# Kernel optimization log

Measured on AMD Instinct MI355X. Metric: run time of the kernel, lower is better.

Reference implementation:

```python
import jax, jax.numpy as jnp
import numpy as np

B, L, C, R, DK = 8, 2048, 512, 64, 64
H = 2 * C  # hdnSize
NEG = -32767.0  # -2**15 + 1
EPS = 1e-5


def _p(key, shape, std=0.02):
    return (jax.random.normal(key, shape, dtype=jnp.float32) * std)


def setup_inputs() -> dict:
    key = jax.random.key(0)
    ks = jax.random.split(key, 16)
    inp = {
        "x": jax.random.normal(ks[0], (B, L, C), dtype=jnp.float32),
        "maskPAD": jax.random.randint(ks[1], (B, 1, L), 0, 2, dtype=jnp.int32),
        "preScores": jax.random.normal(ks[2], (B, R, R), dtype=jnp.float32),
        "Wp": _p(ks[3], (C, R)), "bp": jnp.zeros((R,), jnp.float32),
        "Wq": _p(ks[4], (C, DK)), "bq": jnp.zeros((DK,), jnp.float32),
        "Wk": _p(ks[5], (C, DK)), "bk": jnp.zeros((DK,), jnp.float32),
        "Wv": _p(ks[6], (C, H)), "bv": jnp.zeros((H,), jnp.float32),
        "Wu": _p(ks[7], (C, H)), "bu": jnp.zeros((H,), jnp.float32),
        "Wo": _p(ks[8], (H, C)), "bo": jnp.zeros((C,), jnp.float32),
        "gamma": jnp.ones((C,), jnp.float32),
        "beta": jnp.zeros((C,), jnp.float32),
    }
    return inp


def reference(x, maskPAD, preScores, Wp, bp, Wq, bq, Wk, bk, Wv, bv, Wu, bu, Wo, bo, gamma, beta):
    # GLU gate: [B,L,H]
    gate = jax.nn.silu(x @ Wu + bu)
    # pseudo-attention logits [B,L,r], masked on padded positions
    pScore = x @ Wp + bp
    pad = (maskPAD[:, 0] == 0)[..., None]  # [B,L,1]
    pScore = jnp.where(pad, NEG, pScore)
    pAlpha = jax.nn.softmax(pScore, axis=1)    # softmax over L (dim=-2)
    pAlpha_ = jax.nn.softmax(pScore, axis=-1)  # softmax over r
    # compress: px [B,r,C]  (== pAlpha.transpose(-1,-2) @ x)
    px = jnp.einsum('blr,blc->brc', pAlpha, x)
    q = jax.nn.silu(px @ Wq + bq)  # [B,r,dk]
    k = jax.nn.silu(px @ Wk + bk)  # [B,r,dk]
    v = jax.nn.silu(px @ Wv + bv)  # [B,r,H]
    scores = jnp.einsum('brd,bsd->brs', q, k) / np.sqrt(DK).astype(np.float32)
    scores = scores + preScores
    alpha = jax.nn.softmax(scores, axis=2)
    z = alpha @ v                                # [B,r,H]
    z = jnp.einsum('blr,brh->blh', pAlpha_, z)   # expand back to [B,L,H]
    z = gate * z
    z = z @ Wo + bo                              # [B,L,C]
    y = x + z
    mu = jnp.mean(y, axis=-1, keepdims=True)
    var = jnp.var(y, axis=-1, keepdims=True)
    out = (y - mu) * jax.lax.rsqrt(var + EPS) * gamma + beta
    return out
```

## Files before the change

### kernel.cpp

```cpp
#include <hip/hip_runtime.h>
#include <hip/hip_bf16.h>

constexpr int B_ = 8;
constexpr int L_ = 2048;
constexpr int C_ = 512;
constexpr int R_ = 64;
constexpr int DK_ = 64;
constexpr int H_ = 1024;
constexpr int M_ = B_ * L_;
constexpr int NQKV_ = 1152;
constexpr float NEG_ = -32767.0f;

__device__ __forceinline__ float toF(float x) { return x; }
__device__ __forceinline__ float toF(__hip_bfloat16 x) { return __bfloat162float(x); }
__device__ __forceinline__ float siluf(float v) { return v / (1.0f + __expf(-v)); }
__device__ __forceinline__ ushort bfbits(float f) {
    __hip_bfloat16 h = __float2bfloat16(f);
    union { __hip_bfloat16 h; ushort u; } cv; cv.h = h; return cv.u;
}
__device__ __forceinline__ float bf2f(ushort u) {
    union { uint u; float f; } cv; cv.u = (uint)u << 16; return cv.f;
}

typedef __attribute__((ext_vector_type(8))) short bf16x8;
typedef __attribute__((ext_vector_type(4))) float f32x4;

#define GLOBAL_AS __attribute__((address_space(1)))
#define LDS_AS    __attribute__((address_space(3)))
__device__ __forceinline__ void glds16(const ushort* g, ushort* l) {
    __builtin_amdgcn_global_load_lds((const GLOBAL_AS void*)g, (LDS_AS void*)l, 16, 0, 0);
}

#define VMCNT(n) asm volatile("s_waitcnt vmcnt(" #n ")" ::: "memory")
#define BARRIER() do { __builtin_amdgcn_s_barrier(); asm volatile("" ::: "memory"); } while (0)

template <int EPI>
__global__ __launch_bounds__(256) void mfma_gemm5(
    const ushort* __restrict__ A, const ushort* __restrict__ Bt,
    const float* __restrict__ bias,
    const float* __restrict__ residF, const ushort* __restrict__ residB,
    const int* __restrict__ mask,
    ushort* __restrict__ outB, float* __restrict__ outF, float* __restrict__ outF2,
    int Ndim, int Kdim, int gridN, long bBatch)
{
    __shared__ ushort As[3][128 * 32];
    __shared__ ushort Bs[3][128 * 32];

    const int i = blockIdx.x;
    const int G = gridDim.x >> 3;
    const int gi = (gridDim.x & 7) ? i : ((i & 7) * G + (i >> 3));
    const int nt = gi % gridN, mt = gi / gridN;
    const int m0 = mt * 128, n0 = nt * 128;

    const int tid = threadIdx.x;
    const int lane = tid & 63, w = tid >> 6;
    const int wm = (w & 1) * 64, wn = (w >> 1) * 64;
    const int lr = lane & 15, lq = lane >> 4;

    const int sr = lane >> 2;
    const int sc = (lane & 3) * 8;
    const int s0 = w * 2, s1 = w * 2 + 1;

    const ushort* Bp = Bt + (bBatch ? (long)(m0 / L_) * bBatch : 0);
    int br0 = n0 + s0 * 16 + sr; if (br0 >= Ndim) br0 = Ndim - 1;
    int br1 = n0 + s1 * 16 + sr; if (br1 >= Ndim) br1 = Ndim - 1;
    const ushort* a0p = A  + (size_t)(m0 + s0 * 16 + sr) * Kdim + sc;
    const ushort* a1p = A  + (size_t)(m0 + s1 * 16 + sr) * Kdim + sc;
    const ushort* b0p = Bp + (size_t)br0 * Kdim + sc;
    const ushort* b1p = Bp + (size_t)br1 * Kdim + sc;
    const int lo0 = s0 * 512 + lane * 8;
    const int lo1 = s1 * 512 + lane * 8;

    f32x4 acc[4][4];
#pragma unroll
    for (int a = 0; a < 4; ++a)
#pragma unroll
        for (int b = 0; b < 4; ++b) acc[a][b] = (f32x4){0.f, 0.f, 0.f, 0.f};

    glds16(a0p, &As[0][lo0]);
    glds16(a1p, &As[0][lo1]);
    glds16(b0p, &Bs[0][lo0]);
    glds16(b1p, &Bs[0][lo1]);
    if (32 < Kdim) {
        glds16(a0p + 32, &As[1][lo0]);
        glds16(a1p + 32, &As[1][lo1]);
        glds16(b0p + 32, &Bs[1][lo0]);
        glds16(b1p + 32, &Bs[1][lo1]);
    }

    int cur = 0;
    for (int k0 = 0; k0 < Kdim; k0 += 32) {
        if (k0 + 32 < Kdim) VMCNT(4); else VMCNT(0);
        BARRIER();
        if (k0 + 64 < Kdim) {
            const int nx = cur ? cur - 1 : 2;
            glds16(a0p + k0 + 64, &As[nx][lo0]);
            glds16(a1p + k0 + 64, &As[nx][lo1]);
            glds16(b0p + k0 + 64, &Bs[nx][lo0]);
            glds16(b1p + k0 + 64, &Bs[nx][lo1]);
        }
        bf16x8 af[4], bf[4];
#pragma unroll
        for (int a = 0; a < 4; ++a)
            af[a] = *(const bf16x8*)&As[cur][(wm + a * 16 + lr) * 32 + lq * 8];
#pragma unroll
        for (int b = 0; b < 4; ++b)
            bf[b] = *(const bf16x8*)&Bs[cur][(wn + b * 16 + lr) * 32 + lq * 8];
#pragma unroll
        for (int a = 0; a < 4; ++a)
#pragma unroll
            for (int b = 0; b < 4; ++b)
                acc[a][b] = __builtin_amdgcn_mfma_f32_16x16x32_bf16(af[a], bf[b], acc[a][b], 0, 0, 0);
        cur = (cur == 2) ? 0 : cur + 1;
    }

#pragma unroll
    for (int a = 0; a < 4; ++a) {
#pragma unroll
        for (int b = 0; b < 4; ++b) {
            const int col = n0 + wn + b * 16 + lr;
            if (col < Ndim) {
                const float bn = (EPI == 3) ? 0.f : bias[col];
#pragma unroll
                for (int r = 0; r < 4; ++r) {
                    const int row = m0 + wm + a * 16 + lq * 4 + r;
                    float v = acc[a][b][r];
                    if (EPI == 0) {
                        v = siluf(v + bn);
                        outB[(size_t)row * Ndim + col] = bfbits(v);
                    } else if (EPI == 2) {
                        v += bn + residF[(size_t)row * Ndim + col];
                        outB[(size_t)row * Ndim + col] = bfbits(v);
                    } else {
                        v *= bf2f(residB[(size_t)row * Ndim + col]);
                        outB[(size_t)row * Ndim + col] = bfbits(v);
                    }
                }
            }
        }
    }
}

__global__ __launch_bounds__(256) void pscore_gemm(
    const ushort* __restrict__ x16, const ushort* __restrict__ Wpt,
    const float* __restrict__ bp, const int* __restrict__ mask,
    ushort* __restrict__ pAR16, float* __restrict__ pScoreT)
{
    __shared__ ushort As[3][128 * 32];
    __shared__ ushort Bs[3][64 * 32];

    const int i = blockIdx.x;
    const int G = gridDim.x >> 3;
    const int gi = (i & 7) * G + (i >> 3);
    const int m0 = gi * 128;

    const int tid = threadIdx.x;
    const int lane = tid & 63, w = tid >> 6;
    const int lr = lane & 15, lq = lane >> 4;
    const int sr = lane >> 2, sc = (lane & 3) * 8;
    const int s0 = w * 2, s1 = w * 2 + 1;

    const ushort* a0p = x16 + (size_t)(m0 + s0 * 16 + sr) * C_ + sc;
    const ushort* a1p = x16 + (size_t)(m0 + s1 * 16 + sr) * C_ + sc;
    const ushort* bwp = Wpt + (size_t)(w * 16 + sr) * C_ + sc;
    const int lo0 = s0 * 512 + lane * 8;
    const int lo1 = s1 * 512 + lane * 8;
    const int lob = w * 512 + lane * 8;

    f32x4 acc[2][4];
#pragma unroll
    for (int a = 0; a < 2; ++a)
#pragma unroll
        for (int b = 0; b < 4; ++b) acc[a][b] = (f32x4){0.f, 0.f, 0.f, 0.f};

    glds16(a0p, &As[0][lo0]);
    glds16(a1p, &As[0][lo1]);
    glds16(bwp, &Bs[0][lob]);
    glds16(a0p + 32, &As[1][lo0]);
    glds16(a1p + 32, &As[1][lo1]);
    glds16(bwp + 32, &Bs[1][lob]);

    int cur = 0;
    for (int k0 = 0; k0 < C_; k0 += 32) {
        if (k0 + 32 < C_) VMCNT(3); else VMCNT(0);
        BARRIER();
        if (k0 + 64 < C_) {
            const int nx = cur ? cur - 1 : 2;
            glds16(a0p + k0 + 64, &As[nx][lo0]);
            glds16(a1p + k0 + 64, &As[nx][lo1]);
            glds16(bwp + k0 + 64, &Bs[nx][lob]);
        }
        bf16x8 af[2], bf[4];
#pragma unroll
        for (int a = 0; a < 2; ++a)
            af[a] = *(const bf16x8*)&As[cur][(w * 32 + a * 16 + lr) * 32 + lq * 8];
#pragma unroll
        for (int b = 0; b < 4; ++b)
            bf[b] = *(const bf16x8*)&Bs[cur][(b * 16 + lr) * 32 + lq * 8];
#pragma unroll
        for (int a = 0; a < 2; ++a)
#pragma unroll
            for (int b = 0; b < 4; ++b)
                acc[a][b] = __builtin_amdgcn_mfma_f32_16x16x32_bf16(af[a], bf[b], acc[a][b], 0, 0, 0);
        cur = (cur == 2) ? 0 : cur + 1;
    }

#pragma unroll
    for (int a = 0; a < 2; ++a) {
#pragma unroll
        for (int r = 0; r < 4; ++r) {
            const int row = m0 + w * 32 + a * 16 + lq * 4 + r;
            const bool dead = (mask[row] == 0);
            const int bb = row >> 11, ll = row & (L_ - 1);
            float v[4];
            float mx = -3.4e38f;
#pragma unroll
            for (int b = 0; b < 4; ++b) {
                const int col = b * 16 + lr;
                float t = acc[a][b][r] + bp[col];
                if (dead) t = NEG_;
                v[b] = t;
                pScoreT[((size_t)bb * R_ + col) * L_ + ll] = t;
                mx = fmaxf(mx, t);
            }
#pragma unroll
            for (int o = 1; o < 16; o <<= 1) mx = fmaxf(mx, __shfl_xor(mx, o, 64));
            float e[4], s = 0.f;
#pragma unroll
            for (int b = 0; b < 4; ++b) { e[b] = __expf(v[b] - mx); s += e[b]; }
#pragma unroll
            for (int o = 1; o < 16; o <<= 1) s += __shfl_xor(s, o, 64);
            const float inv = 1.0f / s;
#pragma unroll
            for (int b = 0; b < 4; ++b)
                pAR16[(size_t)row * R_ + b * 16 + lr] = bfbits(e[b] * inv);
        }
    }
}

__global__ __launch_bounds__(256) void fused_gate_z(
    const ushort* __restrict__ x16, const ushort* __restrict__ Wut,
    const float* __restrict__ bu,
    const ushort* __restrict__ pAR, const ushort* __restrict__ zsT,
    ushort* __restrict__ zg)
{
    __shared__ ushort As[2][128 * 32];
    __shared__ ushort Bs[2][128 * 32];

    const int i = blockIdx.x;
    const int G = gridDim.x >> 3;
    const int gi = (i & 7) * G + (i >> 3);
    constexpr int gridN = H_ / 128;
    const int nt = gi % gridN, mt = gi / gridN;
    const int m0 = mt * 128, n0 = nt * 128;

    const int tid = threadIdx.x;
    const int lane = tid & 63, w = tid >> 6;
    const int wm = (w & 1) * 64, wn = (w >> 1) * 64;
    const int lr = lane & 15, lq = lane >> 4;
    const int sr = lane >> 2, sc = (lane & 3) * 8;
    const int s0 = w * 2, s1 = w * 2 + 1;

    const int bidx = m0 >> 11;
    const ushort* a0p = x16 + (size_t)(m0 + s0 * 16 + sr) * C_ + sc;
    const ushort* a1p = x16 + (size_t)(m0 + s1 * 16 + sr) * C_ + sc;
    const ushort* b0p = Wut + (size_t)(n0 + s0 * 16 + sr) * C_ + sc;
    const ushort* b1p = Wut + (size_t)(n0 + s1 * 16 + sr) * C_ + sc;
    const ushort* zb  = zsT + (size_t)bidx * H_ * R_;
    const ushort* c0p = pAR + (size_t)(m0 + s0 * 16 + sr) * R_ + sc;
    const ushort* c1p = pAR + (size_t)(m0 + s1 * 16 + sr) * R_ + sc;
    const ushort* d0p = zb + (size_t)(n0 + s0 * 16 + sr) * R_ + sc;
    const ushort* d1p = zb + (size_t)(n0 + s1 * 16 + sr) * R_ + sc;
    const int lo0 = s0 * 512 + lane * 8;
    const int lo1 = s1 * 512 + lane * 8;

    f32x4 acc[4][4];
#pragma unroll
    for (int a = 0; a < 4; ++a)
#pragma unroll
        for (int b = 0; b < 4; ++b) acc[a][b] = (f32x4){0.f, 0.f, 0.f, 0.f};

    glds16(c0p, &As[0][lo0]);
    glds16(c1p, &As[0][lo1]);
    glds16(d0p, &Bs[0][lo0]);
    glds16(d1p, &Bs[0][lo1]);

    int cur = 0;
#pragma unroll
    for (int kt = 0; kt < 2; ++kt) {
        __syncthreads();
        if (kt == 0) {
            glds16(c0p + 32, &As[1][lo0]);
            glds16(c1p + 32, &As[1][lo1]);
            glds16(d0p + 32, &Bs[1][lo0]);
            glds16(d1p + 32, &Bs[1][lo1]);
        } else {
            glds16(a0p, &As[0][lo0]);
            glds16(a1p, &As[0][lo1]);
            glds16(b0p, &Bs[0][lo0]);
            glds16(b1p, &Bs[0][lo1]);
        }
        bf16x8 af[4], bf[4];
#pragma unroll
        for (int a = 0; a < 4; ++a)
            af[a] = *(const bf16x8*)&As[cur][(wm + a * 16 + lr) * 32 + lq * 8];
#pragma unroll
        for (int b = 0; b < 4; ++b)
            bf[b] = *(const bf16x8*)&Bs[cur][(wn + b * 16 + lr) * 32 + lq * 8];
#pragma unroll
        for (int a = 0; a < 4; ++a)
#pragma unroll
            for (int b = 0; b < 4; ++b)
                acc[a][b] = __builtin_amdgcn_mfma_f32_16x16x32_bf16(af[a], bf[b], acc[a][b], 0, 0, 0);
        cur ^= 1;
    }

    uint pk[4][4][2];
#pragma unroll
    for (int a = 0; a < 4; ++a)
#pragma unroll
        for (int b = 0; b < 4; ++b) {
            pk[a][b][0] = (uint)bfbits(acc[a][b][0]) | ((uint)bfbits(acc[a][b][1]) << 16);
            pk[a][b][1] = (uint)bfbits(acc[a][b][2]) | ((uint)bfbits(acc[a][b][3]) << 16);
            acc[a][b] = (f32x4){0.f, 0.f, 0.f, 0.f};
        }

    for (int k0 = 0; k0 < C_; k0 += 32) {
        __syncthreads();
        if (k0 + 32 < C_) {
            const int nx = cur ^ 1;
            glds16(a0p + k0 + 32, &As[nx][lo0]);
            glds16(a1p + k0 + 32, &As[nx][lo1]);
            glds16(b0p + k0 + 32, &Bs[nx][lo0]);
            glds16(b1p + k0 + 32, &Bs[nx][lo1]);
        }
        bf16x8 af[4], bf[4];
#pragma unroll
        for (int a = 0; a < 4; ++a)
            af[a] = *(const bf16x8*)&As[cur][(wm + a * 16 + lr) * 32 + lq * 8];
#pragma unroll
        for (int b = 0; b < 4; ++b)
            bf[b] = *(const bf16x8*)&Bs[cur][(wn + b * 16 + lr) * 32 + lq * 8];
#pragma unroll
        for (int a = 0; a < 4; ++a)
#pragma unroll
            for (int b = 0; b < 4; ++b)
                acc[a][b] = __builtin_amdgcn_mfma_f32_16x16x32_bf16(af[a], bf[b], acc[a][b], 0, 0, 0);
        cur ^= 1;
    }

#pragma unroll
    for (int a = 0; a < 4; ++a) {
#pragma unroll
        for (int b = 0; b < 4; ++b) {
            const int col = n0 + wn + b * 16 + lr;
            const float bn = bu[col];
#pragma unroll
            for (int r = 0; r < 4; ++r) {
                const int row = m0 + wm + a * 16 + lq * 4 + r;
                const ushort zu = (ushort)((r & 1) ? (pk[a][b][r >> 1] >> 16)
                                                   : (pk[a][b][r >> 1] & 0xffff));
                const float v = siluf(acc[a][b][r] + bn) * bf2f(zu);
                zg[(size_t)row * H_ + col] = bfbits(v);
            }
        }
    }
}

__global__ __launch_bounds__(256) void x_prep(const float* __restrict__ x,
                                              ushort* __restrict__ x16,
                                              ushort* __restrict__ xT16)
{
    __shared__ float tile[32][33];
    const int tx = threadIdx.x & 31, ty = threadIdx.x >> 5;
    const int c0 = blockIdx.x * 32, l0 = blockIdx.y * 32;
#pragma unroll
    for (int i = 0; i < 32; i += 8) {
        const float v = x[(size_t)(l0 + ty + i) * C_ + c0 + tx];
        tile[ty + i][tx] = v;
        x16[(size_t)(l0 + ty + i) * C_ + c0 + tx] = bfbits(v);
    }
    __syncthreads();
    const int bb = l0 >> 11, ll0 = l0 & (L_ - 1);
#pragma unroll
    for (int i = 0; i < 32; i += 8)
        xT16[((size_t)bb * C_ + c0 + ty + i) * L_ + ll0 + tx] = bfbits(tile[tx][ty + i]);
}

__global__ __launch_bounds__(256) void prep_w(
    const float* __restrict__ Wu, const float* __restrict__ Wo, const float* __restrict__ Wp,
    const float* __restrict__ Wq, const float* __restrict__ bq,
    const float* __restrict__ Wk, const float* __restrict__ bk,
    const float* __restrict__ Wv, const float* __restrict__ bv,
    ushort* __restrict__ Wut, ushort* __restrict__ Wot, ushort* __restrict__ Wpt,
    ushort* __restrict__ Wqkvt, float* __restrict__ bqkv)
{
    int id = blockIdx.x;
    const float* W; ushort* Wt; const float* bsrc = nullptr;
    int K, Nloc, n0, k0, nn0;
    if (id < 512) {
        W = Wu; Wt = Wut; K = 512; Nloc = 1024;
        n0 = (id & 31) * 32; k0 = (id >> 5) * 32; nn0 = n0;
    } else if (id < 1024) {
        id -= 512; W = Wo; Wt = Wot; K = 1024; Nloc = 512;
        n0 = (id & 15) * 32; k0 = (id >> 4) * 32; nn0 = n0;
    } else if (id < 1056) {
        id -= 1024; W = Wp; Wt = Wpt; K = 512; Nloc = 64;
        n0 = (id & 1) * 32; k0 = (id >> 1) * 32; nn0 = n0;
    } else {
        id -= 1056; K = 512; Wt = Wqkvt;
        n0 = (id % 36) * 32; k0 = (id / 36) * 32;
        if (n0 < 64)       { W = Wq; bsrc = bq; Nloc = 64;   nn0 = n0; }
        else if (n0 < 128) { W = Wk; bsrc = bk; Nloc = 64;   nn0 = n0 - 64; }
        else               { W = Wv; bsrc = bv; Nloc = 1024; nn0 = n0 - 128; }
    }
    __shared__ float tile[32][33];
    const int tx = threadIdx.x & 31, ty = threadIdx.x >> 5;
#pragma unroll
    for (int i = 0; i < 32; i += 8)
        tile[ty + i][tx] = W[(size_t)(k0 + ty + i) * Nloc + nn0 + tx];
    __syncthreads();
#pragma unroll
    for (int i = 0; i < 32; i += 8)
        Wt[(size_t)(n0 + ty + i) * K + k0 + tx] = bfbits(tile[tx][ty + i]);
    if (bsrc && k0 == 0 && threadIdx.x < 32) bqkv[n0 + threadIdx.x] = bsrc[nn0 + threadIdx.x];
}

__global__ __launch_bounds__(256) void softmaxL2(const float* __restrict__ pScoreT,
                                                 ushort* __restrict__ pALT)
{
    const size_t br = blockIdx.x;
    const float* row = pScoreT + br * L_;
    ushort* orow = pALT + br * L_;
    const int t = threadIdx.x;
    __shared__ float red[256];

    float v[8];
    float mx = -3.4e38f;
#pragma unroll
    for (int j = 0; j < 8; ++j) { v[j] = row[t + j * 256]; mx = fmaxf(mx, v[j]); }
    red[t] = mx; __syncthreads();
    for (int s = 128; s > 0; s >>= 1) { if (t < s) red[t] = fmaxf(red[t], red[t + s]); __syncthreads(); }
    mx = red[0]; __syncthreads();

    float e[8], sum = 0.f;
#pragma unroll
    for (int j = 0; j < 8; ++j) { e[j] = __expf(v[j] - mx); sum += e[j]; }
    red[t] = sum; __syncthreads();
    for (int s = 128; s > 0; s >>= 1) { if (t < s) red[t] += red[t + s]; __syncthreads(); }
    const float inv = 1.0f / red[0];
#pragma unroll
    for (int j = 0; j < 8; ++j) orow[t + j * 256] = bfbits(e[j] * inv);
}

__global__ __launch_bounds__(512) void compress_mfma(
    const ushort* __restrict__ pALT, const ushort* __restrict__ xT,
    float* __restrict__ parts)
{
    __shared__ ushort As[3][64 * 32];
    __shared__ ushort Bs[3][256 * 32];

    const int bidx = blockIdx.y;
    const int n0 = blockIdx.x * 256;
    const int ks = blockIdx.z;
    const int kbeg = ks * (L_ / 4), kend = kbeg + L_ / 4;
    const int tid = threadIdx.x;
    const int lane = tid & 63, w = tid >> 6;
    const int lr = lane & 15, lq = lane >> 4;
    const int sr = lane >> 2, sc = (lane & 3) * 8;
    const int wm = (w & 1) * 32, wn = (w >> 1) * 64;

    const ushort* Ab = pALT + (size_t)bidx * R_ * L_;
    const ushort* Bb = xT + (size_t)bidx * C_ * L_;

    const int aseg = (w >= 4) ? (w - 4) : 0;
    const ushort* ap = Ab + (size_t)(aseg * 16 + sr) * L_ + sc;
    const int alo = aseg * 512 + lane * 8;
    const ushort* b0p = Bb + (size_t)(n0 + (w * 2) * 16 + sr) * L_ + sc;
    const ushort* b1p = Bb + (size_t)(n0 + (w * 2 + 1) * 16 + sr) * L_ + sc;
    const int blo0 = (w * 2) * 512 + lane * 8;
    const int blo1 = (w * 2 + 1) * 512 + lane * 8;

    auto stage = [&](int k0, int bsel) {
        if (w >= 4) glds16(ap + k0, &As[bsel][alo]);
        glds16(b0p + k0, &Bs[bsel][blo0]);
        glds16(b1p + k0, &Bs[bsel][blo1]);
    };

    f32x4 acc[2][4];
#pragma unroll
    for (int a = 0; a < 2; ++a)
#pragma unroll
        for (int b = 0; b < 4; ++b) acc[a][b] = (f32x4){0.f, 0.f, 0.f, 0.f};

    stage(kbeg, 0);
    stage(kbeg + 32, 1);

    int cur = 0;
    for (int k0 = kbeg; k0 < kend; k0 += 32) {
        if (k0 + 32 < kend) {
            if (w >= 4) VMCNT(3); else VMCNT(2);
        } else {
            VMCNT(0);
        }
        BARRIER();
        if (k0 + 64 < kend) stage(k0 + 64, cur ? cur - 1 : 2);
        bf16x8 af[2], bf[4];
#pragma unroll
        for (int a = 0; a < 2; ++a)
            af[a] = *(const bf16x8*)&As[cur][(wm + a * 16 + lr) * 32 + lq * 8];
#pragma unroll
        for (int b = 0; b < 4; ++b)
            bf[b] = *(const bf16x8*)&Bs[cur][(wn + b * 16 + lr) * 32 + lq * 8];
#pragma unroll
        for (int a = 0; a < 2; ++a)
#pragma unroll
            for (int b = 0; b < 4; ++b)
                acc[a][b] = __builtin_amdgcn_mfma_f32_16x16x32_bf16(af[a], bf[b], acc[a][b], 0, 0, 0);
        cur = (cur == 2) ? 0 : cur + 1;
    }
#pragma unroll
    for (int a = 0; a < 2; ++a)
#pragma unroll
        for (int b = 0; b < 4; ++b)
#pragma unroll
            for (int r = 0; r < 4; ++r) {
                const int row = wm + a * 16 + lq * 4 + r;
                const int col = n0 + wn + b * 16 + lr;
                parts[(((size_t)ks * B_ + bidx) * R_ + row) * C_ + col] = acc[a][b][r];
            }
}

__global__ __launch_bounds__(256) void compress_reduce16(const float* __restrict__ parts,
                                                         ushort* __restrict__ px16)
{
    const size_t i = ((size_t)blockIdx.x * 256 + threadIdx.x) * 4;
    constexpr size_t S = (size_t)B_ * R_ * C_;
    const float4 a = *(const float4*)(parts + i);
    const float4 b = *(const float4*)(parts + i + S);
    const float4 c = *(const float4*)(parts + i + 2 * S);
    const float4 d = *(const float4*)(parts + i + 3 * S);
    ushort4 o;
    o.x = bfbits(a.x + b.x + c.x + d.x);
    o.y = bfbits(a.y + b.y + c.y + d.y);
    o.z = bfbits(a.z + b.z + c.z + d.z);
    o.w = bfbits(a.w + b.w + c.w + d.w);
    *(ushort4*)(px16 + i) = o;
}

__global__ __launch_bounds__(256) void attn_fused(
    const ushort* __restrict__ qkv, const float* __restrict__ preS,
    ushort* __restrict__ zsT)
{
    const int b = blockIdx.x >> 6, r = blockIdx.x & 63;
    const int t = threadIdx.x;
    __shared__ float al[R_];
    if (t < 64) {
        const ushort* qr = qkv + (size_t)(b * R_ + r) * NQKV_;
        const ushort* ks = qkv + (size_t)(b * R_ + t) * NQKV_ + 64;
        float acc = 0.f;
#pragma unroll
        for (int d = 0; d < DK_; d += 4) {
            const ushort4 qa = *(const ushort4*)(qr + d);
            const ushort4 ka = *(const ushort4*)(ks + d);
            acc += bf2f(qa.x) * bf2f(ka.x) + bf2f(qa.y) * bf2f(ka.y)
                 + bf2f(qa.z) * bf2f(ka.z) + bf2f(qa.w) * bf2f(ka.w);
        }
        acc = acc * 0.125f + preS[((size_t)b * R_ + r) * R_ + t];
        float mx = acc;
#pragma unroll
        for (int o = 32; o > 0; o >>= 1) mx = fmaxf(mx, __shfl_xor(mx, o, 64));
        float e = __expf(acc - mx);
        float sm = e;
#pragma unroll
        for (int o = 32; o > 0; o >>= 1) sm += __shfl_xor(sm, o, 64);
        al[t] = e / sm;
    }
    __syncthreads();
    float acc[4] = {};
    for (int s = 0; s < R_; ++s) {
        const float a = al[s];
        const ushort* vr = qkv + (size_t)(b * R_ + s) * NQKV_ + 128;
#pragma unroll
        for (int j = 0; j < 4; ++j) acc[j] += a * bf2f(vr[t + j * 256]);
    }
#pragma unroll
    for (int j = 0; j < 4; ++j) {
        const int h = t + j * 256;
        zsT[((size_t)b * H_ + h) * R_ + r] = bfbits(acc[j]);
    }
}

__global__ __launch_bounds__(256) void layernorm(const ushort* __restrict__ y,
                                                 const float* __restrict__ gamma,
                                                 const float* __restrict__ beta,
                                                 float* __restrict__ out)
{
    const size_t m = blockIdx.x;
    const int t = threadIdx.x;
    const ushort2 p = *(const ushort2*)(y + m * C_ + 2 * t);
    float v0 = bf2f(p.x), v1 = bf2f(p.y);
    __shared__ float rs[256], rq[256];
    rs[t] = v0 + v1;
    rq[t] = v0 * v0 + v1 * v1;
    __syncthreads();
    for (int o = 128; o > 0; o >>= 1) {
        if (t < o) { rs[t] += rs[t + o]; rq[t] += rq[t + o]; }
        __syncthreads();
    }
    const float mu = rs[0] * (1.0f / C_);
    const float var = rq[0] * (1.0f / C_) - mu * mu;
    const float inv = rsqrtf(var + 1e-5f);
    const float2 g = *(const float2*)(gamma + 2 * t);
    const float2 be = *(const float2*)(beta + 2 * t);
    float2 o;
    o.x = (v0 - mu) * inv * g.x + be.x;
    o.y = (v1 - mu) * inv * g.y + be.y;
    *(float2*)(out + m * C_ + 2 * t) = o;
}

template <typename AT, typename BT, typename RT, int ACT, int EPI>
__global__ __launch_bounds__(256) void gemm64(
    const AT* __restrict__ A, const BT* __restrict__ Bw,
    const float* __restrict__ bias, const int* __restrict__ mask,
    const RT* resid, float* __restrict__ outF, __hip_bfloat16* outB,
    int Ndim, int Kdim, long bBatchStride)
{
    __shared__ float As[16][68];
    __shared__ float Bs[16][64];
    const int tid = threadIdx.x;
    const int tx = tid & 15, ty = tid >> 4;
    const int n0 = blockIdx.x * 64, m0 = blockIdx.y * 64;
    const BT* Bp = Bw + (bBatchStride ? (long)(m0 / L_) * bBatchStride : 0);
    float acc[4][4] = {};
    for (int k0 = 0; k0 < Kdim; k0 += 16) {
#pragma unroll
        for (int s = 0; s < 4; ++s) {
            int idx = tid + s * 256;
            int am = idx >> 4, ak = idx & 15;
            As[ak][am] = toF(A[(size_t)(m0 + am) * Kdim + k0 + ak]);
        }
#pragma unroll
        for (int s = 0; s < 4; ++s) {
            int idx = tid + s * 256;
            int bk = idx >> 6, bn = idx & 63;
            Bs[bk][bn] = toF(Bp[(size_t)(k0 + bk) * Ndim + n0 + bn]);
        }
        __syncthreads();
#pragma unroll
        for (int kk = 0; kk < 16; ++kk) {
            float av[4], bv[4];
            *(float4*)av = *(const float4*)&As[kk][ty * 4];
            *(float4*)bv = *(const float4*)&Bs[kk][tx * 4];
#pragma unroll
            for (int i = 0; i < 4; ++i)
#pragma unroll
                for (int j = 0; j < 4; ++j) acc[i][j] += av[i] * bv[j];
        }
        __syncthreads();
    }
#pragma unroll
    for (int i = 0; i < 4; ++i) {
        int m = m0 + ty * 4 + i;
#pragma unroll
        for (int j = 0; j < 4; ++j) {
            int n = n0 + tx * 4 + j;
            float val = acc[i][j];
            if (EPI != 3) val += bias[n];
            if (ACT) val = siluf(val);
            if (EPI == 0) outB[(size_t)m * Ndim + n] = __float2bfloat16(val);
            else if (EPI == 1) { if (mask[m] == 0) val = NEG_; outF[(size_t)m * Ndim + n] = val; }
            else if (EPI == 2) { val += toF(resid[(size_t)m * Ndim + n]); outB[(size_t)m * Ndim + n] = __float2bfloat16(val); }
            else { val *= toF(resid[(size_t)m * Ndim + n]); outB[(size_t)m * Ndim + n] = __float2bfloat16(val); }
        }
    }
}

template <int OUT>
__global__ __launch_bounds__(64) void softmaxR(const float* __restrict__ pScore,
                                               float* __restrict__ outF,
                                               ushort* __restrict__ outU)
{
    const size_t m = blockIdx.x;
    const int t = threadIdx.x;
    float v = pScore[m * R_ + t];
    float mx = v;
#pragma unroll
    for (int o = 32; o > 0; o >>= 1) mx = fmaxf(mx, __shfl_xor(mx, o, 64));
    float e = __expf(v - mx);
    float s = e;
#pragma unroll
    for (int o = 32; o > 0; o >>= 1) s += __shfl_xor(s, o, 64);
    if (OUT == 0) outF[m * R_ + t] = e / s;
    else          outU[m * R_ + t] = bfbits(e / s);
}

__global__ __launch_bounds__(256) void softmaxL(const float* __restrict__ pScore,
                                                float* __restrict__ pAlpha)
{
    const int b = blockIdx.x >> 6, r = blockIdx.x & 63;
    const int t = threadIdx.x;
    const float* base = pScore + (size_t)b * L_ * R_ + r;
    float* out = pAlpha + (size_t)b * L_ * R_ + r;
    __shared__ float red[256];
    float mx = -3.4e38f;
    for (int l = t; l < L_; l += 256) mx = fmaxf(mx, base[(size_t)l * R_]);
    red[t] = mx; __syncthreads();
    for (int s = 128; s > 0; s >>= 1) { if (t < s) red[t] = fmaxf(red[t], red[t + s]); __syncthreads(); }
    mx = red[0]; __syncthreads();
    float sum = 0.f;
    for (int l = t; l < L_; l += 256) {
        float e = __expf(base[(size_t)l * R_] - mx);
        out[(size_t)l * R_] = e; sum += e;
    }
    red[t] = sum; __syncthreads();
    for (int s = 128; s > 0; s >>= 1) { if (t < s) red[t] += red[t + s]; __syncthreads(); }
    const float inv = 1.0f / red[0];
    for (int l = t; l < L_; l += 256) out[(size_t)l * R_] *= inv;
}

__global__ __launch_bounds__(256) void compress_part(
    const float* __restrict__ pAlpha, const float* __restrict__ x,
    float* __restrict__ parts)
{
    __shared__ float As[16][64];
    __shared__ float Bs[16][64];
    const int tid = threadIdx.x;
    const int tx = tid & 15, ty = tid >> 4;
    const int n0 = blockIdx.x * 64;
    const int ks = blockIdx.y;
    const int b  = blockIdx.z;
    const float* pa = pAlpha + (size_t)b * L_ * R_;
    const float* xb = x + (size_t)b * L_ * C_;
    float acc[4][4] = {};
    const int kbeg = ks * (L_ / 4), kend = kbeg + L_ / 4;
    for (int k0 = kbeg; k0 < kend; k0 += 16) {
#pragma unroll
        for (int s = 0; s < 4; ++s) {
            int idx = tid + s * 256;
            int kk = idx >> 6, m = idx & 63;
            As[kk][m] = pa[(size_t)(k0 + kk) * R_ + m];
        }
#pragma unroll
        for (int s = 0; s < 4; ++s) {
            int idx = tid + s * 256;
            int kk = idx >> 6, n = idx & 63;
            Bs[kk][n] = xb[(size_t)(k0 + kk) * C_ + n0 + n];
        }
        __syncthreads();
#pragma unroll
        for (int kk = 0; kk < 16; ++kk) {
            float av[4], bv[4];
            *(float4*)av = *(const float4*)&As[kk][ty * 4];
            *(float4*)bv = *(const float4*)&Bs[kk][tx * 4];
#pragma unroll
            for (int i = 0; i < 4; ++i)
#pragma unroll
                for (int j = 0; j < 4; ++j) acc[i][j] += av[i] * bv[j];
        }
        __syncthreads();
    }
#pragma unroll
    for (int i = 0; i < 4; ++i)
#pragma unroll
        for (int j = 0; j < 4; ++j)
            parts[((((size_t)ks * B_ + b) * R_) + ty * 4 + i) * C_ + n0 + tx * 4 + j] = acc[i][j];
}

__global__ __launch_bounds__(256) void compress_reduce(const float* __restrict__ parts,
                                                       float* __restrict__ px)
{
    const size_t i = (size_t)blockIdx.x * 256 + threadIdx.x;
    constexpr size_t S = (size_t)B_ * R_ * C_;
    px[i] = parts[i] + parts[i + S] + parts[i + 2 * S] + parts[i + 3 * S];
}

__global__ __launch_bounds__(256) void qkv_gemm(
    const float* __restrict__ px,
    const float* __restrict__ Wq, const float* __restrict__ bq,
    const float* __restrict__ Wk, const float* __restrict__ bk,
    const float* __restrict__ Wv, const float* __restrict__ bv,
    float* __restrict__ q, float* __restrict__ k, float* __restrict__ v)
{
    __shared__ float As[16][68];
    __shared__ float Bs[16][64];
    const int tid = threadIdx.x;
    const int tx = tid & 15, ty = tid >> 4;
    const int bx = blockIdx.x;
    const int m0 = blockIdx.y * 64;
    const float* W; const float* bias; float* dst; int Nloc, ncol0;
    if (bx == 0)      { W = Wq; bias = bq; dst = q; Nloc = 64;   ncol0 = 0; }
    else if (bx == 1) { W = Wk; bias = bk; dst = k; Nloc = 64;   ncol0 = 0; }
    else              { W = Wv; bias = bv; dst = v; Nloc = H_;   ncol0 = (bx - 2) * 64; }

    float acc[4][4] = {};
    for (int k0 = 0; k0 < C_; k0 += 16) {
#pragma unroll
        for (int s = 0; s < 4; ++s) {
            int idx = tid + s * 256;
            int am = idx >> 4, ak = idx & 15;
            As[ak][am] = px[(size_t)(m0 + am) * C_ + k0 + ak];
        }
#pragma unroll
        for (int s = 0; s < 4; ++s) {
            int idx = tid + s * 256;
            int kk = idx >> 6, bn = idx & 63;
            Bs[kk][bn] = W[(size_t)(k0 + kk) * Nloc + ncol0 + bn];
        }
        __syncthreads();
#pragma unroll
        for (int kk = 0; kk < 16; ++kk) {
            float av[4], bv4[4];
            *(float4*)av = *(const float4*)&As[kk][ty * 4];
            *(float4*)bv4 = *(const float4*)&Bs[kk][tx * 4];
#pragma unroll
            for (int i = 0; i < 4; ++i)
#pragma unroll
                for (int j = 0; j < 4; ++j) acc[i][j] += av[i] * bv4[j];
        }
        __syncthreads();
    }
#pragma unroll
    for (int i = 0; i < 4; ++i) {
        int m = m0 + ty * 4 + i;
#pragma unroll
        for (int j = 0; j < 4; ++j) {
            int n = ncol0 + tx * 4 + j;
            dst[(size_t)m * Nloc + n] = siluf(acc[i][j] + bias[n]);
        }
    }
}

template <int MODE>
__global__ __launch_bounds__(256) void attn_z(const float* __restrict__ alpha,
                                              const float* __restrict__ v,
                                              float* __restrict__ zsF,
                                              ushort* __restrict__ zsT)
{
    const int b = blockIdx.x >> 6, r = blockIdx.x & 63;
    const int t = threadIdx.x;
    __shared__ float al[R_];
    if (t < R_) al[t] = alpha[((size_t)b * R_ + r) * R_ + t];
    __syncthreads();
    float acc[4] = {};
    for (int s = 0; s < R_; ++s) {
        float a = al[s];
        const float* vr = v + ((size_t)b * R_ + s) * H_;
#pragma unroll
        for (int j = 0; j < 4; ++j) acc[j] += a * vr[t + j * 256];
    }
#pragma unroll
    for (int j = 0; j < 4; ++j) {
        const int h = t + j * 256;
        if (MODE == 0) zsF[((size_t)b * R_ + r) * H_ + h] = acc[j];
        else           zsT[((size_t)b * H_ + h) * R_ + r] = bfbits(acc[j]);
    }
}

__global__ __launch_bounds__(64) void attn_scores(
    const float* __restrict__ q, const float* __restrict__ k,
    const float* __restrict__ preS, float* __restrict__ alpha)
{
    const int b = blockIdx.x >> 6, r = blockIdx.x & 63;
    const int s = threadIdx.x;
    const float* qr = q + ((size_t)b * R_ + r) * DK_;
    const float* ks = k + ((size_t)b * R_ + s) * DK_;
    float acc = 0.f;
#pragma unroll
    for (int d = 0; d < DK_; ++d) acc += qr[d] * ks[d];
    acc = acc * 0.125f + preS[((size_t)b * R_ + r) * R_ + s];
    float mx = acc;
#pragma unroll
    for (int o = 32; o > 0; o >>= 1) mx = fmaxf(mx, __shfl_xor(mx, o, 64));
    float e = __expf(acc - mx);
    float sm = e;
#pragma unroll
    for (int o = 32; o > 0; o >>= 1) sm += __shfl_xor(sm, o, 64);
    alpha[((size_t)b * R_ + r) * R_ + s] = e / sm;
}

extern "C" void kernel_launch(void* const* d_in, const int* in_sizes, int n_in,
                              void* d_out, int out_size, void* d_ws, size_t ws_size,
                              hipStream_t stream)
{
    using bf16 = __hip_bfloat16;
    const float* x      = (const float*)d_in[0];
    const int*  maskPAD = (const int*)d_in[1];
    const float* preS   = (const float*)d_in[2];
    const float* Wp     = (const float*)d_in[3];
    const float* bp     = (const float*)d_in[4];
    const float* Wq     = (const float*)d_in[5];
    const float* bq     = (const float*)d_in[6];
    const float* Wk     = (const float*)d_in[7];
    const float* bk     = (const float*)d_in[8];
    const float* Wv     = (const float*)d_in[9];
    const float* bv     = (const float*)d_in[10];
    const float* Wu     = (const float*)d_in[11];
    const float* bu     = (const float*)d_in[12];
    const float* Wo     = (const float*)d_in[13];
    const float* bo     = (const float*)d_in[14];
    const float* gamma  = (const float*)d_in[15];
    const float* beta   = (const float*)d_in[16];
    float* out          = (float*)d_out;

    char* ws = (char*)d_ws;
    const bool bigWS = ws_size >= (size_t)52 * 1024 * 1024;

    if (bigWS) {
        bf16* zg = (bf16*)ws;
        float* parts = (float*)ws;
        char* pool = ws + (size_t)M_ * H_ * 2;
        float* pScoreT = (float*)pool;
        ushort* pALT   = (ushort*)(pScoreT + (size_t)B_ * R_ * L_);
        ushort* pAR16  = pALT + (size_t)B_ * R_ * L_;
        ushort* px16   = pAR16 + (size_t)M_ * R_;
        ushort* qkv16  = px16 + (size_t)B_ * R_ * C_;
        ushort* zsT16  = qkv16 + (size_t)B_ * R_ * NQKV_;
        ushort* Wqkvt  = zsT16 + (size_t)B_ * H_ * R_;
        float*  bqkv   = (float*)(Wqkvt + (size_t)NQKV_ * C_);
        bf16*  y       = (bf16*)pool;
        ushort* Wut    = (ushort*)(pool + 18221568);
        ushort* Wot    = Wut + (size_t)C_ * H_;
        ushort* Wpt    = Wot + (size_t)C_ * H_;
        ushort* x16    = (ushort*)d_out;
        ushort* xT16   = x16 + (size_t)M_ * C_;

        x_prep<<<dim3(C_ / 32, M_ / 32), 256, 0, stream>>>(x, x16, xT16);
        prep_w<<<1632, 256, 0, stream>>>(Wu, Wo, Wp, Wq, bq, Wk, bk, Wv, bv,
                                         Wut, Wot, Wpt, Wqkvt, bqkv);
        pscore_gemm<<<M_ / 128, 256, 0, stream>>>(x16, Wpt, bp, maskPAD, pAR16, pScoreT);
        softmaxL2<<<B_ * R_, 256, 0, stream>>>(pScoreT, pALT);
        compress_mfma<<<dim3(C_ / 256, B_, 4), 512, 0, stream>>>(pALT, xT16, parts);
        compress_reduce16<<<(B_ * R_ * C_) / 1024, 256, 0, stream>>>(parts, px16);
        mfma_gemm5<0><<<(NQKV_ / 128) * ((B_ * R_) / 128), 256, 0, stream>>>(
            px16, Wqkvt, bqkv, nullptr, nullptr, nullptr, qkv16, nullptr, nullptr,
            NQKV_, C_, NQKV_ / 128, 0);
        attn_fused<<<B_ * R_, 256, 0, stream>>>(qkv16, preS, zsT16);
        fused_gate_z<<<(H_ / 128) * (M_ / 128), 256, 0, stream>>>(
            x16, Wut, bu, pAR16, zsT16, (ushort*)zg);
        mfma_gemm5<2><<<(C_ / 128) * (M_ / 128), 256, 0, stream>>>(
            (ushort*)zg, Wot, bo, x, nullptr, nullptr, (ushort*)y, nullptr, nullptr,
            C_, H_, C_ / 128, 0);
        layernorm<<<M_, 256, 0, stream>>>((const ushort*)y, gamma, beta, out);
    } else {
        float* pScore = (float*)ws;
        float* pAL   = pScore + (size_t)M_ * R_;
        float* pAR   = pAL    + (size_t)M_ * R_;
        float* px    = pAR    + (size_t)M_ * R_;
        float* q     = px     + (size_t)B_ * R_ * C_;
        float* kk    = q      + (size_t)B_ * R_ * DK_;
        float* vv    = kk     + (size_t)B_ * R_ * DK_;
        float* alpha = vv     + (size_t)B_ * R_ * H_;
        float* zs    = alpha  + (size_t)B_ * R_ * R_;
        bf16* gate_b = (bf16*)(zs + (size_t)B_ * R_ * H_);
        bf16* y_b    = (bf16*)((char*)gate_b + (size_t)L_ * H_ * 2);

        gemm64<float, float, float, 0, 1><<<dim3(R_ / 64, M_ / 64), 256, 0, stream>>>(
            x, Wp, bp, maskPAD, (const float*)nullptr, pScore, nullptr, R_, C_, 0);
        softmaxL<<<B_ * R_, 256, 0, stream>>>(pScore, pAL);
        softmaxR<0><<<M_, 64, 0, stream>>>(pScore, pAR, nullptr);
        compress_part<<<dim3(C_ / 64, 4, B_), 256, 0, stream>>>(pAL, x, pScore);
        compress_reduce<<<(B_ * R_ * C_) / 256, 256, 0, stream>>>(pScore, px);
        qkv_gemm<<<dim3(2 + H_ / 64, (B_ * R_) / 64), 256, 0, stream>>>(
            px, Wq, bq, Wk, bk, Wv, bv, q, kk, vv);
        attn_scores<<<B_ * R_, 64, 0, stream>>>(q, kk, preS, alpha);
        attn_z<0><<<B_ * R_, 256, 0, stream>>>(alpha, vv, zs, nullptr);

        for (int b = 0; b < B_; ++b) {
            const float* xb = x + (size_t)b * L_ * C_;
            gemm64<float, float, float, 1, 0><<<dim3(H_ / 64, L_ / 64), 256, 0, stream>>>(
                xb, Wu, bu, nullptr, (const float*)nullptr, nullptr, gate_b, H_, C_, 0);
            gemm64<float, float, bf16, 0, 3><<<dim3(H_ / 64, L_ / 64), 256, 0, stream>>>(
                pAR + (size_t)b * L_ * R_, zs + (size_t)b * R_ * H_,
                nullptr, nullptr, gate_b, nullptr, gate_b, H_, R_, 0);
            gemm64<bf16, float, float, 0, 2><<<dim3(C_ / 64, L_ / 64), 256, 0, stream>>>(
                gate_b, Wo, bo, nullptr, xb, nullptr, y_b, C_, H_, 0);
            layernorm<<<L_, 256, 0, stream>>>((const ushort*)y_b, gamma, beta, out + (size_t)b * L_ * C_);
        }
    }
}
```

Baseline: 271.4 us.

## Use 256x128 tiles with 512-thread blocks for gate and output GEMMs

The fused gate/z kernel and the output projection GEMM now use 256-row by 128-column tiles with 8 waves per block instead of 128x128 tiles with 4 waves. Each B-tile row is loaded once per wave, which raises reuse of the weight tile across more rows and halves the number of blocks. The gate kernel's two-phase loop is merged into one 18-step staged loop through a lambda. The trade-off is more LDS per block and fewer blocks in flight, which could lower occupancy or wave balance.

```diff
diff --git a/kernel.cpp b/kernel.cpp
--- a/kernel.cpp
+++ b/kernel.cpp
@@ -141,6 +141,87 @@
     }
 }
 
+template <int EPI>
+__global__ __launch_bounds__(512, 4) void gemm256(
+    const ushort* __restrict__ A, const ushort* __restrict__ Bt,
+    const float* __restrict__ bias, const float* __restrict__ residF,
+    ushort* __restrict__ outB, int Ndim, int Kdim, int gridN)
+{
+    __shared__ ushort As[2][256 * 32];
+    __shared__ ushort Bs[2][128 * 32];
+
+    const int i = blockIdx.x;
+    const int G = gridDim.x >> 3;
+    const int gi = (gridDim.x & 7) ? i : ((i & 7) * G + (i >> 3));
+    const int nt = gi % gridN, mt = gi / gridN;
+    const int m0 = mt * 256, n0 = nt * 128;
+
+    const int tid = threadIdx.x;
+    const int lane = tid & 63, w = tid >> 6;
+    const int wm = (w & 3) * 64, wn = (w >> 2) * 64;
+    const int lr = lane & 15, lq = lane >> 4;
+    const int sr = lane >> 2, sc = (lane & 3) * 8;
+    const int s0 = w * 2, s1 = w * 2 + 1;
+
+    const ushort* a0p = A + (size_t)(m0 + s0 * 16 + sr) * Kdim + sc;
+    const ushort* a1p = A + (size_t)(m0 + s1 * 16 + sr) * Kdim + sc;
+    const ushort* b0p = Bt + (size_t)(n0 + w * 16 + sr) * Kdim + sc;
+    const int lo0 = s0 * 512 + lane * 8;
+    const int lo1 = s1 * 512 + lane * 8;
+    const int lob = w * 512 + lane * 8;
+
+    f32x4 acc[4][4];
+#pragma unroll
+    for (int a = 0; a < 4; ++a)
+#pragma unroll
+        for (int b = 0; b < 4; ++b) acc[a][b] = (f32x4){0.f, 0.f, 0.f, 0.f};
+
+    glds16(a0p, &As[0][lo0]);
+    glds16(a1p, &As[0][lo1]);
+    glds16(b0p, &Bs[0][lob]);
+
+    int cur = 0;
+    for (int k0 = 0; k0 < Kdim; k0 += 32) {
+        __syncthreads();
+        if (k0 + 32 < Kdim) {
+            const int nx = cur ^ 1;
+            glds16(a0p + k0 + 32, &As[nx][lo0]);
+            glds16(a1p + k0 + 32, &As[nx][lo1]);
+            glds16(b0p + k0 + 32, &Bs[nx][lob]);
+        }
+        bf16x8 af[4], bf[4];
+#pragma unroll
+        for (int a = 0; a < 4; ++a)
+            af[a] = *(const bf16x8*)&As[cur][(wm + a * 16 + lr) * 32 + lq * 8];
+#pragma unroll
+        for (int b = 0; b < 4; ++b)
+            bf[b] = *(const bf16x8*)&Bs[cur][(wn + b * 16 + lr) * 32 + lq * 8];
+#pragma unroll
+        for (int a = 0; a < 4; ++a)
+#pragma unroll
+            for (int b = 0; b < 4; ++b)
+                acc[a][b] = __builtin_amdgcn_mfma_f32_16x16x32_bf16(af[a], bf[b], acc[a][b], 0, 0, 0);
+        cur ^= 1;
+    }
+
+#pragma unroll
+    for (int a = 0; a < 4; ++a) {
+#pragma unroll
+        for (int b = 0; b < 4; ++b) {
+            const int col = n0 + wn + b * 16 + lr;
+            const float bn = bias[col];
+#pragma unroll
+            for (int r = 0; r < 4; ++r) {
+                const int row = m0 + wm + a * 16 + lq * 4 + r;
+                float v = acc[a][b][r] + bn;
+                if (EPI == 2) v += residF[(size_t)row * Ndim + col];
+                else if (EPI == 0) v = siluf(v);
+                outB[(size_t)row * Ndim + col] = bfbits(v);
+            }
+        }
+    }
+}
+
 __global__ __launch_bounds__(256) void pscore_gemm(
     const ushort* __restrict__ x16, const ushort* __restrict__ Wpt,
     const float* __restrict__ bp, const int* __restrict__ mask,
@@ -238,13 +319,13 @@
     }
 }
 
-__global__ __launch_bounds__(256) void fused_gate_z(
+__global__ __launch_bounds__(512, 4) void fused_gate_z(
     const ushort* __restrict__ x16, const ushort* __restrict__ Wut,
     const float* __restrict__ bu,
     const ushort* __restrict__ pAR, const ushort* __restrict__ zsT,
     ushort* __restrict__ zg)
 {
-    __shared__ ushort As[2][128 * 32];
+    __shared__ ushort As[2][256 * 32];
     __shared__ ushort Bs[2][128 * 32];
 
     const int i = blockIdx.x;
@@ -252,11 +333,11 @@
     const int gi = (i & 7) * G + (i >> 3);
     constexpr int gridN = H_ / 128;
     const int nt = gi % gridN, mt = gi / gridN;
-    const int m0 = mt * 128, n0 = nt * 128;
+    const int m0 = mt * 256, n0 = nt * 128;
 
     const int tid = threadIdx.x;
     const int lane = tid & 63, w = tid >> 6;
-    const int wm = (w & 1) * 64, wn = (w >> 1) * 64;
+    const int wm = (w & 3) * 64, wn = (w >> 2) * 64;
     const int lr = lane & 15, lq = lane >> 4;
     const int sr = lane >> 2, sc = (lane & 3) * 8;
     const int s0 = w * 2, s1 = w * 2 + 1;
@@ -264,15 +345,28 @@
     const int bidx = m0 >> 11;
     const ushort* a0p = x16 + (size_t)(m0 + s0 * 16 + sr) * C_ + sc;
     const ushort* a1p = x16 + (size_t)(m0 + s1 * 16 + sr) * C_ + sc;
-    const ushort* b0p = Wut + (size_t)(n0 + s0 * 16 + sr) * C_ + sc;
-    const ushort* b1p = Wut + (size_t)(n0 + s1 * 16 + sr) * C_ + sc;
+    const ushort* b0p = Wut + (size_t)(n0 + w * 16 + sr) * C_ + sc;
     const ushort* zb  = zsT + (size_t)bidx * H_ * R_;
     const ushort* c0p = pAR + (size_t)(m0 + s0 * 16 + sr) * R_ + sc;
     const ushort* c1p = pAR + (size_t)(m0 + s1 * 16 + sr) * R_ + sc;
-    const ushort* d0p = zb + (size_t)(n0 + s0 * 16 + sr) * R_ + sc;
-    const ushort* d1p = zb + (size_t)(n0 + s1 * 16 + sr) * R_ + sc;
+    const ushort* d0p = zb + (size_t)(n0 + w * 16 + sr) * R_ + sc;
     const int lo0 = s0 * 512 + lane * 8;
     const int lo1 = s1 * 512 + lane * 8;
+    const int lob = w * 512 + lane * 8;
+
+    auto stage = [&](int t, int bsel) {
+        if (t < 2) {
+            const int off = t * 32;
+            glds16(c0p + off, &As[bsel][lo0]);
+            glds16(c1p + off, &As[bsel][lo1]);
+            glds16(d0p + off, &Bs[bsel][lob]);
+        } else {
+            const int off = (t - 2) * 32;
+            glds16(a0p + off, &As[bsel][lo0]);
+            glds16(a1p + off, &As[bsel][lo1]);
+            glds16(b0p + off, &Bs[bsel][lob]);
+        }
+    };
 
     f32x4 acc[4][4];
 #pragma unroll
@@ -280,26 +374,14 @@
 #pragma unroll
         for (int b = 0; b < 4; ++b) acc[a][b] = (f32x4){0.f, 0.f, 0.f, 0.f};
 
-    glds16(c0p, &As[0][lo0]);
-    glds16(c1p, &As[0][lo1]);
-    glds16(d0p, &Bs[0][lo0]);
-    glds16(d1p, &Bs[0][lo1]);
+    uint pk[4][4][2];
+
+    stage(0, 0);
 
     int cur = 0;
-#pragma unroll
-    for (int kt = 0; kt < 2; ++kt) {
+    for (int t = 0; t < 18; ++t) {
         __syncthreads();
-        if (kt == 0) {
-            glds16(c0p + 32, &As[1][lo0]);
-            glds16(c1p + 32, &As[1][lo1]);
-            glds16(d0p + 32, &Bs[1][lo0]);
-            glds16(d1p + 32, &Bs[1][lo1]);
-        } else {
-            glds16(a0p, &As[0][lo0]);
-            glds16(a1p, &As[0][lo1]);
-            glds16(b0p, &Bs[0][lo0]);
-            glds16(b1p, &Bs[0][lo1]);
-        }
+        if (t + 1 < 18) stage(t + 1, cur ^ 1);
         bf16x8 af[4], bf[4];
 #pragma unroll
         for (int a = 0; a < 4; ++a)
@@ -312,40 +394,16 @@
 #pragma unroll
             for (int b = 0; b < 4; ++b)
                 acc[a][b] = __builtin_amdgcn_mfma_f32_16x16x32_bf16(af[a], bf[b], acc[a][b], 0, 0, 0);
-        cur ^= 1;
-    }
-
-    uint pk[4][4][2];
-#pragma unroll
-    for (int a = 0; a < 4; ++a)
-#pragma unroll
-        for (int b = 0; b < 4; ++b) {
-            pk[a][b][0] = (uint)bfbits(acc[a][b][0]) | ((uint)bfbits(acc[a][b][1]) << 16);
-            pk[a][b][1] = (uint)bfbits(acc[a][b][2]) | ((uint)bfbits(acc[a][b][3]) << 16);
-            acc[a][b] = (f32x4){0.f, 0.f, 0.f, 0.f};
-        }
-
-    for (int k0 = 0; k0 < C_; k0 += 32) {
-        __syncthreads();
-        if (k0 + 32 < C_) {
-            const int nx = cur ^ 1;
-            glds16(a0p + k0 + 32, &As[nx][lo0]);
-            glds16(a1p + k0 + 32, &As[nx][lo1]);
-            glds16(b0p + k0 + 32, &Bs[nx][lo0]);
-            glds16(b1p + k0 + 32, &Bs[nx][lo1]);
-        }
-        bf16x8 af[4], bf[4];
-#pragma unroll
-        for (int a = 0; a < 4; ++a)
-            af[a] = *(const bf16x8*)&As[cur][(wm + a * 16 + lr) * 32 + lq * 8];
-#pragma unroll
-        for (int b = 0; b < 4; ++b)
-            bf[b] = *(const bf16x8*)&Bs[cur][(wn + b * 16 + lr) * 32 + lq * 8];
-#pragma unroll
-        for (int a = 0; a < 4; ++a)
-#pragma unroll
-            for (int b = 0; b < 4; ++b)
-                acc[a][b] = __builtin_amdgcn_mfma_f32_16x16x32_bf16(af[a], bf[b], acc[a][b], 0, 0, 0);
+        if (t == 1) {
+#pragma unroll
+            for (int a = 0; a < 4; ++a)
+#pragma unroll
+                for (int b = 0; b < 4; ++b) {
+                    pk[a][b][0] = (uint)bfbits(acc[a][b][0]) | ((uint)bfbits(acc[a][b][1]) << 16);
+                    pk[a][b][1] = (uint)bfbits(acc[a][b][2]) | ((uint)bfbits(acc[a][b][3]) << 16);
+                    acc[a][b] = (f32x4){0.f, 0.f, 0.f, 0.f};
+                }
+        }
         cur ^= 1;
     }
 
@@ -936,11 +994,10 @@
             px16, Wqkvt, bqkv, nullptr, nullptr, nullptr, qkv16, nullptr, nullptr,
             NQKV_, C_, NQKV_ / 128, 0);
         attn_fused<<<B_ * R_, 256, 0, stream>>>(qkv16, preS, zsT16);
-        fused_gate_z<<<(H_ / 128) * (M_ / 128), 256, 0, stream>>>(
+        fused_gate_z<<<(H_ / 128) * (M_ / 256), 512, 0, stream>>>(
             x16, Wut, bu, pAR16, zsT16, (ushort*)zg);
-        mfma_gemm5<2><<<(C_ / 128) * (M_ / 128), 256, 0, stream>>>(
-            (ushort*)zg, Wot, bo, x, nullptr, nullptr, (ushort*)y, nullptr, nullptr,
-            C_, H_, C_ / 128, 0);
+        gemm256<2><<<(C_ / 128) * (M_ / 256), 512, 0, stream>>>(
+            (ushort*)zg, Wot, bo, x, (ushort*)y, C_, H_, C_ / 128);
         layernorm<<<M_, 256, 0, stream>>>((const ushort*)y, gamma, beta, out);
     } else {
         float* pScore = (float*)ws;
```

Measured after the change: 285.6 us. +5.2%, slower.
